# Kernel optimization log

Hardware: AMD Instinct MI355X
Metric: run time of the kernel (lower is better)

## Reference

```python
import jax, jax.numpy as jnp
import numpy as np

N_NODES = 50000
N_EDGES = 1600000
IN_CH = 128
OUT_CH = 32
HEADS = 4
NEG_SLOPE = 0.2

def setup_inputs() -> dict:
    key = jax.random.key(0)
    ks = jax.random.split(key, 6)
    x = jax.random.normal(ks[0], (N_NODES, IN_CH), dtype=jnp.float32)
    edge_index = jax.random.randint(ks[1], (2, N_EDGES), 0, N_NODES, dtype=jnp.int64)
    # GATConv parameters (glorot-ish scale)
    W = jax.random.normal(ks[2], (IN_CH, HEADS * OUT_CH), dtype=jnp.float32) * (1.0 / np.sqrt(IN_CH))
    att_src = jax.random.normal(ks[3], (HEADS, OUT_CH), dtype=jnp.float32) * (1.0 / np.sqrt(OUT_CH))
    att_dst = jax.random.normal(ks[4], (HEADS, OUT_CH), dtype=jnp.float32) * (1.0 / np.sqrt(OUT_CH))
    bias = jnp.zeros((HEADS * OUT_CH,), dtype=jnp.float32)
    return {"x": x, "edge_index": edge_index, "W": W, "att_src": att_src, "att_dst": att_dst, "bias": bias}

def reference(x, edge_index, W, att_src, att_dst, bias):
    N = x.shape[0]
    H, C = att_src.shape
    # PyG default: add self loops
    loop = jnp.arange(N, dtype=edge_index.dtype)
    src = jnp.concatenate([edge_index[0], loop])  # [E+N]
    dst = jnp.concatenate([edge_index[1], loop])  # [E+N]
    # linear projection -> [N, H, C]
    h = (x @ W).reshape(N, H, C)
    # per-node attention contributions [N, H]
    a_src = jnp.einsum('nhc,hc->nh', h, att_src)
    a_dst = jnp.einsum('nhc,hc->nh', h, att_dst)
    # edge-wise logits with LeakyReLU [E', H]
    alpha = jax.nn.leaky_relu(a_src[src] + a_dst[dst], negative_slope=NEG_SLOPE)
    # segment softmax over incoming edges of each dst node
    amax = jax.ops.segment_max(alpha, dst, num_segments=N)
    alpha = jnp.exp(alpha - amax[dst])
    denom = jax.ops.segment_sum(alpha, dst, num_segments=N)
    alpha = alpha / (denom[dst] + 1e-16)
    # weighted scatter-aggregate of source features [N, H, C]
    msg = h[src] * alpha[..., None]
    out = jax.ops.segment_sum(msg, dst, num_segments=N)
    out = out.reshape(N, H * C) + bias  # concat heads + bias
    return out, alpha
```

## Files before the change

### kernel.cpp

```cpp
#include <hip/hip_runtime.h>
#include <math.h>

#define N_NODES 50000
#define N_EDGES 1600000
#define E_TOT   1650000
#define GROWS   32
#define GEMM_BLOCKS ((N_NODES + GROWS - 1) / GROWS)
#define STRIDE  72
#define NBKT    391
#define PPART   450
#define EPB     3556
#define CAP     32

__device__ __forceinline__ unsigned short f2bf(float f) {
    unsigned int b = __float_as_uint(f);
    return (unsigned short)((b + 0x7FFFu + ((b >> 16) & 1u)) >> 16);
}
__device__ __forceinline__ float bf_lo(unsigned int u) {
    return __uint_as_float(u << 16);
}
__device__ __forceinline__ float bf_hi(unsigned int u) {
    return __uint_as_float(u & 0xFFFF0000u);
}

__global__ __launch_bounds__(256) void k_gemm_part(
    const float* __restrict__ x, const float* __restrict__ W,
    const float* __restrict__ att_src, const float* __restrict__ att_dst,
    unsigned short* __restrict__ hbuf16, float* __restrict__ asrc,
    float* __restrict__ adst,
    const int* __restrict__ esrc, const int* __restrict__ edst,
    unsigned int* __restrict__ cells, int* __restrict__ cellCnt)
{
    __shared__ float  xs[GROWS * 128];
    __shared__ float4 Wl[64 * 32];
    __shared__ int    cur[NBKT];
    const int tid = threadIdx.x;

    if (blockIdx.x >= PPART) {
        const int n0 = (blockIdx.x - PPART) * GROWS;

        {
            const float4* xg = (const float4*)x;
            float4* xs4 = (float4*)xs;
            #pragma unroll
            for (int i = 0; i < 4; i++) {
                int idx = tid + 256 * i;
                int row = n0 + (idx >> 5);
                int col = idx & 31;
                row = min(row, N_NODES - 1);
                xs4[idx] = xg[(size_t)row * 32 + col];
            }
        }

        const int ct = tid & 31;
        const int rt = tid >> 5;
        const int rb = rt * 4;

        float acc[4][4];
        #pragma unroll
        for (int r = 0; r < 4; r++)
            #pragma unroll
            for (int q = 0; q < 4; q++) acc[r][q] = 0.f;

        const float4* W4 = (const float4*)W;
        #pragma unroll
        for (int kc = 0; kc < 2; kc++) {
            const float4* Wg = W4 + kc * 2048;
            __syncthreads();
            #pragma unroll
            for (int i = 0; i < 8; i++)
                Wl[tid + 256 * i] = Wg[tid + 256 * i];
            __syncthreads();

            const int kb = kc * 64;
            #pragma unroll 4
            for (int k = 0; k < 64; k++) {
                float4 wv = Wl[k * 32 + ct];
                #pragma unroll
                for (int r = 0; r < 4; r++) {
                    float xr = xs[(rb + r) * 128 + kb + k];
                    acc[r][0] = fmaf(xr, wv.x, acc[r][0]);
                    acc[r][1] = fmaf(xr, wv.y, acc[r][1]);
                    acc[r][2] = fmaf(xr, wv.z, acc[r][2]);
                    acc[r][3] = fmaf(xr, wv.w, acc[r][3]);
                }
            }
        }

        ushort4* h4 = (ushort4*)hbuf16;
        #pragma unroll
        for (int r = 0; r < 4; r++) {
            int row = n0 + rb + r;
            if (row < N_NODES) {
                ushort4 p;
                p.x = f2bf(acc[r][0]); p.y = f2bf(acc[r][1]);
                p.z = f2bf(acc[r][2]); p.w = f2bf(acc[r][3]);
                h4[(size_t)row * 32 + ct] = p;
            }
        }

        const int head = ct >> 3;
        const int c0   = (ct & 7) * 4;
        const float* As = att_src + head * 32 + c0;
        const float* Ad = att_dst + head * 32 + c0;
        float sv[4], dv[4];
        #pragma unroll
        for (int r = 0; r < 4; r++) {
            sv[r] = acc[r][0]*As[0] + acc[r][1]*As[1] + acc[r][2]*As[2] + acc[r][3]*As[3];
            dv[r] = acc[r][0]*Ad[0] + acc[r][1]*Ad[1] + acc[r][2]*Ad[2] + acc[r][3]*Ad[3];
        }
        #pragma unroll
        for (int off = 4; off >= 1; off >>= 1) {
            #pragma unroll
            for (int r = 0; r < 4; r++) {
                sv[r] += __shfl_down(sv[r], off, 8);
                dv[r] += __shfl_down(dv[r], off, 8);
            }
        }
        if ((ct & 7) == 0) {
            #pragma unroll
            for (int r = 0; r < 4; r++) {
                int row = n0 + rb + r;
                if (row < N_NODES) {
                    asrc[row * 4 + head] = sv[r];
                    adst[row * 4 + head] = dv[r];
                }
            }
        }
    } else {
        const int p = blockIdx.x;
        for (int i = tid; i < NBKT; i += 256) cur[i] = 0;
        __syncthreads();

        const int base = p * EPB;
        const int end  = min(base + EPB, N_EDGES);
        unsigned int* myCells = cells + (size_t)p * NBKT * CAP;
        for (int e = base + tid; e < end; e += 256) {
            int d = edst[e];
            int s = esrc[e];
            int bkt = d >> 7;
            int pos = atomicAdd(&cur[bkt], 1);
            if (pos < CAP)
                myCells[bkt * CAP + pos] = ((unsigned int)(d & 127) << 16) | (unsigned int)s;
        }
        __syncthreads();
        for (int i = tid; i < NBKT; i += 256)
            cellCnt[p * NBKT + i] = min(cur[i], CAP);
    }
}

__global__ __launch_bounds__(512) void k_build(
    const unsigned int* __restrict__ cells, const int* __restrict__ cellCnt,
    int* __restrict__ csr, int* __restrict__ cnt)
{
    __shared__ int cur[128];
    __shared__ int scnt[PPART];
    __shared__ __align__(16) int rows[128 * STRIDE];

    const int tid = threadIdx.x;
    const int b   = blockIdx.x;
    const int d0  = b * 128;
    const int ndst = min(128, N_NODES - d0);
    for (int i = tid; i < 128; i += 512) cur[i] = 0;
    for (int i = tid; i < PPART; i += 512) scnt[i] = cellCnt[i * NBKT + b];
    __syncthreads();

    for (int slot = tid; slot < PPART * CAP; slot += 512) {
        int p = slot >> 5;
        int j = slot & 31;
        if (j < scnt[p]) {
            unsigned int v = cells[((size_t)p * NBKT + b) * CAP + j];
            int dlo = (int)(v >> 16);
            int s   = (int)(v & 0xFFFFu);
            int r = atomicAdd(&cur[dlo], 1);
            if (r < STRIDE) rows[dlo * STRIDE + r] = s;
        }
    }
    __syncthreads();

    int4* dst4 = (int4*)(csr + (size_t)d0 * STRIDE);
    const int4* src4 = (const int4*)rows;
    const int n4 = ndst * (STRIDE / 4);
    for (int k = tid; k < n4; k += 512) dst4[k] = src4[k];
    for (int t = tid; t < ndst; t += 512) cnt[d0 + t] = min(cur[t], STRIDE);
}

__global__ __launch_bounds__(64) void k_gather(
    const int* __restrict__ csr, const float4* __restrict__ asrc,
    const float4* __restrict__ adst, const uint4* __restrict__ hbuf4,
    const int* __restrict__ cnt, const float* __restrict__ bias,
    float4* __restrict__ rden, float4* __restrict__ out4)
{
    __shared__ float4 lds_ex[STRIDE + 1];
    __shared__ int    lds_s[STRIDE + 1];

    const int d    = blockIdx.x;
    const int tid  = threadIdx.x;
    const int c    = cnt[d];
    const int ctot = c + 1;
    const float4 b4 = adst[d];
    const int* row = csr + (size_t)d * STRIDE;

    float4 dp = make_float4(0.f, 0.f, 0.f, 0.f);

    for (int i = tid; i < ctot; i += 64) {
        int s = (i < c) ? row[i] : d;
        float4 a4 = asrc[s];
        float l0=a4.x+b4.x, l1=a4.y+b4.y, l2=a4.z+b4.z, l3=a4.w+b4.w;
        l0=fmaxf(l0,0.2f*l0); l1=fmaxf(l1,0.2f*l1);
        l2=fmaxf(l2,0.2f*l2); l3=fmaxf(l3,0.2f*l3);
        float4 ex;
        ex.x=__expf(l0); ex.y=__expf(l1); ex.z=__expf(l2); ex.w=__expf(l3);
        lds_ex[i] = ex;
        lds_s[i]  = s;
        dp.x+=ex.x; dp.y+=ex.y; dp.z+=ex.z; dp.w+=ex.w;
    }

    #pragma unroll
    for (int o = 32; o >= 1; o >>= 1) {
        dp.x += __shfl_down(dp.x, o, 64);
        dp.y += __shfl_down(dp.y, o, 64);
        dp.z += __shfl_down(dp.z, o, 64);
        dp.w += __shfl_down(dp.w, o, 64);
    }
    float rx = 1.0f / (__shfl(dp.x, 0, 64) + 1e-16f);
    float ry = 1.0f / (__shfl(dp.y, 0, 64) + 1e-16f);
    float rz = 1.0f / (__shfl(dp.z, 0, 64) + 1e-16f);
    float rw = 1.0f / (__shfl(dp.w, 0, 64) + 1e-16f);
    if (tid == 0) rden[d] = make_float4(rx, ry, rz, rw);
    __syncthreads();

    const int lane16 = tid & 15;
    const int q      = tid >> 4;
    const int head   = lane16 >> 2;
    const float rh = (head == 0) ? rx : (head == 1) ? ry : (head == 2) ? rz : rw;

    float a0=0.f,a1=0.f,a2=0.f,a3=0.f,a4=0.f,a5=0.f,a6=0.f,a7=0.f;
    for (int j = q; j < ctot; j += 4) {
        float w = ((const float*)&lds_ex[j])[head] * rh;
        int   s = lds_s[j];
        uint4 hv = hbuf4[(size_t)s * 16 + lane16];
        a0 = fmaf(w, bf_lo(hv.x), a0);
        a1 = fmaf(w, bf_hi(hv.x), a1);
        a2 = fmaf(w, bf_lo(hv.y), a2);
        a3 = fmaf(w, bf_hi(hv.y), a3);
        a4 = fmaf(w, bf_lo(hv.z), a4);
        a5 = fmaf(w, bf_hi(hv.z), a5);
        a6 = fmaf(w, bf_lo(hv.w), a6);
        a7 = fmaf(w, bf_hi(hv.w), a7);
    }
    a0 += __shfl_down(a0, 32, 64); a1 += __shfl_down(a1, 32, 64);
    a2 += __shfl_down(a2, 32, 64); a3 += __shfl_down(a3, 32, 64);
    a4 += __shfl_down(a4, 32, 64); a5 += __shfl_down(a5, 32, 64);
    a6 += __shfl_down(a6, 32, 64); a7 += __shfl_down(a7, 32, 64);
    a0 += __shfl_down(a0, 16, 64); a1 += __shfl_down(a1, 16, 64);
    a2 += __shfl_down(a2, 16, 64); a3 += __shfl_down(a3, 16, 64);
    a4 += __shfl_down(a4, 16, 64); a5 += __shfl_down(a5, 16, 64);
    a6 += __shfl_down(a6, 16, 64); a7 += __shfl_down(a7, 16, 64);
    if (tid < 16) {
        float4 bb0 = ((const float4*)bias)[lane16 * 2];
        float4 bb1 = ((const float4*)bias)[lane16 * 2 + 1];
        float4 o0, o1;
        o0.x = a0 + bb0.x; o0.y = a1 + bb0.y; o0.z = a2 + bb0.z; o0.w = a3 + bb0.w;
        o1.x = a4 + bb1.x; o1.y = a5 + bb1.y; o1.z = a6 + bb1.z; o1.w = a7 + bb1.w;
        out4[(size_t)d * 32 + lane16 * 2]     = o0;
        out4[(size_t)d * 32 + lane16 * 2 + 1] = o1;
    }
}

__global__ __launch_bounds__(256) void k_alpha(
    const int* __restrict__ esrc, const int* __restrict__ edst,
    const float4* __restrict__ asrc, const float4* __restrict__ adst,
    const float4* __restrict__ rden, float4* __restrict__ alpha)
{
    int e = blockIdx.x * 256 + threadIdx.x;
    if (e >= E_TOT) return;
    int s, d;
    if (e < N_EDGES) { s = esrc[e]; d = edst[e]; }
    else             { s = e - N_EDGES; d = s; }
    float4 a4 = asrc[s];
    float4 b4 = adst[d];
    float4 r4 = rden[d];
    float l0=a4.x+b4.x, l1=a4.y+b4.y, l2=a4.z+b4.z, l3=a4.w+b4.w;
    l0=fmaxf(l0,0.2f*l0); l1=fmaxf(l1,0.2f*l1);
    l2=fmaxf(l2,0.2f*l2); l3=fmaxf(l3,0.2f*l3);
    float4 w;
    w.x = __expf(l0) * r4.x;
    w.y = __expf(l1) * r4.y;
    w.z = __expf(l2) * r4.z;
    w.w = __expf(l3) * r4.w;
    alpha[e] = w;
}

extern "C" void kernel_launch(void* const* d_in, const int* in_sizes, int n_in,
                              void* d_out, int out_size, void* d_ws, size_t ws_size,
                              hipStream_t stream)
{
    const float* x       = (const float*)d_in[0];
    const int*   ei      = (const int*)d_in[1];
    const float* W       = (const float*)d_in[2];
    const float* att_src = (const float*)d_in[3];
    const float* att_dst = (const float*)d_in[4];
    const float* bias    = (const float*)d_in[5];

    const int* esrc = ei;
    const int* edst = ei + N_EDGES;

    float* out   = (float*)d_out;
    float* alpha = out + (size_t)N_NODES * 128;

    unsigned short* hbuf16 = (unsigned short*)d_ws;
    float* asrc  = (float*)(hbuf16 + (size_t)N_NODES * 128);
    float* adst  = asrc + N_NODES * 4;
    float* rden  = adst + N_NODES * 4;
    int*   cnt   = (int*)(rden + N_NODES * 4);
    int*   csr   = cnt + N_NODES;
    unsigned int* cells = (unsigned int*)(csr + (size_t)N_NODES * STRIDE);
    int*   cellCnt = (int*)(cells + (size_t)PPART * NBKT * CAP);

    k_gemm_part<<<PPART + GEMM_BLOCKS, 256, 0, stream>>>(
        x, W, att_src, att_dst, hbuf16, asrc, adst,
        esrc, edst, cells, cellCnt);

    k_build<<<NBKT, 512, 0, stream>>>(cells, cellCnt, csr, cnt);

    k_gather<<<N_NODES, 64, 0, stream>>>(csr, (const float4*)asrc,
                                         (const float4*)adst,
                                         (const uint4*)hbuf16, cnt, bias,
                                         (float4*)rden, (float4*)out);

    k_alpha<<<(E_TOT + 255) / 256, 256, 0, stream>>>(esrc, edst,
                                                     (const float4*)asrc,
                                                     (const float4*)adst,
                                                     (const float4*)rden,
                                                     (float4*)alpha);
}
```

Baseline: 220.5 us.

## Compute softmax denominators in build, fuse alpha write into gather launch

Measured after the change: 223.4 us. No clear change (+1.4%).

```diff
diff --git a/kernel.cpp b/kernel.cpp
--- a/kernel.cpp
+++ b/kernel.cpp
@@ -11,6 +11,7 @@
 #define PPART   450
 #define EPB     3556
 #define CAP     32
+#define NALPHA  ((E_TOT + 255) / 256)
 
 __device__ __forceinline__ unsigned short f2bf(float f) {
     unsigned int b = __float_as_uint(f);
@@ -62,7 +63,8 @@
             #pragma unroll
             for (int q = 0; q < 4; q++) acc[r][q] = 0.f;
 
-        const float4* W4 = (const float4*)W;
+        const float4* W4  = (const float4*)W;
+        const float4* xs4 = (const float4*)xs;
         #pragma unroll
         for (int kc = 0; kc < 2; kc++) {
             const float4* Wg = W4 + kc * 2048;
@@ -72,17 +74,32 @@
                 Wl[tid + 256 * i] = Wg[tid + 256 * i];
             __syncthreads();
 
-            const int kb = kc * 64;
-            #pragma unroll 4
-            for (int k = 0; k < 64; k++) {
-                float4 wv = Wl[k * 32 + ct];
+            const int kq = kc * 16;
+            #pragma unroll 2
+            for (int k4 = 0; k4 < 16; k4++) {
+                float4 w0 = Wl[(k4 * 4 + 0) * 32 + ct];
+                float4 w1 = Wl[(k4 * 4 + 1) * 32 + ct];
+                float4 w2 = Wl[(k4 * 4 + 2) * 32 + ct];
+                float4 w3 = Wl[(k4 * 4 + 3) * 32 + ct];
                 #pragma unroll
                 for (int r = 0; r < 4; r++) {
-                    float xr = xs[(rb + r) * 128 + kb + k];
-                    acc[r][0] = fmaf(xr, wv.x, acc[r][0]);
-                    acc[r][1] = fmaf(xr, wv.y, acc[r][1]);
-                    acc[r][2] = fmaf(xr, wv.z, acc[r][2]);
-                    acc[r][3] = fmaf(xr, wv.w, acc[r][3]);
+                    float4 xv = xs4[(rb + r) * 32 + kq + k4];
+                    acc[r][0] = fmaf(xv.x, w0.x, acc[r][0]);
+                    acc[r][1] = fmaf(xv.x, w0.y, acc[r][1]);
+                    acc[r][2] = fmaf(xv.x, w0.z, acc[r][2]);
+                    acc[r][3] = fmaf(xv.x, w0.w, acc[r][3]);
+                    acc[r][0] = fmaf(xv.y, w1.x, acc[r][0]);
+                    acc[r][1] = fmaf(xv.y, w1.y, acc[r][1]);
+                    acc[r][2] = fmaf(xv.y, w1.z, acc[r][2]);
+                    acc[r][3] = fmaf(xv.y, w1.w, acc[r][3]);
+                    acc[r][0] = fmaf(xv.z, w2.x, acc[r][0]);
+                    acc[r][1] = fmaf(xv.z, w2.y, acc[r][1]);
+                    acc[r][2] = fmaf(xv.z, w2.z, acc[r][2]);
+                    acc[r][3] = fmaf(xv.z, w2.w, acc[r][3]);
+                    acc[r][0] = fmaf(xv.w, w3.x, acc[r][0]);
+                    acc[r][1] = fmaf(xv.w, w3.y, acc[r][1]);
+                    acc[r][2] = fmaf(xv.w, w3.z, acc[r][2]);
+                    acc[r][3] = fmaf(xv.w, w3.w, acc[r][3]);
                 }
             }
         }
@@ -151,7 +168,8 @@
 
 __global__ __launch_bounds__(512) void k_build(
     const unsigned int* __restrict__ cells, const int* __restrict__ cellCnt,
-    int* __restrict__ csr, int* __restrict__ cnt)
+    const float4* __restrict__ asrc, const float4* __restrict__ adst,
+    int* __restrict__ csr, int* __restrict__ cnt, float4* __restrict__ rden)
 {
     __shared__ int cur[128];
     __shared__ int scnt[PPART];
@@ -183,25 +201,85 @@
     const int n4 = ndst * (STRIDE / 4);
     for (int k = tid; k < n4; k += 512) dst4[k] = src4[k];
     for (int t = tid; t < ndst; t += 512) cnt[d0 + t] = min(cur[t], STRIDE);
-}
-
-__global__ __launch_bounds__(64) void k_gather(
-    const int* __restrict__ csr, const float4* __restrict__ asrc,
+
+    const int g = tid >> 5, l = tid & 31;
+    for (int dd = g; dd < ndst; dd += 16) {
+        const int dn = d0 + dd;
+        const float4 b4 = adst[dn];
+        const int c = min(cur[dd], STRIDE);
+        float4 dp = make_float4(0.f, 0.f, 0.f, 0.f);
+        for (int i = l; i <= c; i += 32) {
+            int s = (i < c) ? rows[dd * STRIDE + i] : dn;
+            float4 a4 = asrc[s];
+            float l0=a4.x+b4.x, l1=a4.y+b4.y, l2=a4.z+b4.z, l3=a4.w+b4.w;
+            l0=fmaxf(l0,0.2f*l0); l1=fmaxf(l1,0.2f*l1);
+            l2=fmaxf(l2,0.2f*l2); l3=fmaxf(l3,0.2f*l3);
+            dp.x += __expf(l0); dp.y += __expf(l1);
+            dp.z += __expf(l2); dp.w += __expf(l3);
+        }
+        #pragma unroll
+        for (int o = 16; o >= 1; o >>= 1) {
+            dp.x += __shfl_down(dp.x, o, 32);
+            dp.y += __shfl_down(dp.y, o, 32);
+            dp.z += __shfl_down(dp.z, o, 32);
+            dp.w += __shfl_down(dp.w, o, 32);
+        }
+        if (l == 0) {
+            float4 r;
+            r.x = 1.0f / (dp.x + 1e-16f);
+            r.y = 1.0f / (dp.y + 1e-16f);
+            r.z = 1.0f / (dp.z + 1e-16f);
+            r.w = 1.0f / (dp.w + 1e-16f);
+            rden[dn] = r;
+        }
+    }
+}
+
+__global__ __launch_bounds__(64) void k_gather_alpha(
+    const int* __restrict__ csr, const int* __restrict__ esrc,
+    const int* __restrict__ edst, const float4* __restrict__ asrc,
     const float4* __restrict__ adst, const uint4* __restrict__ hbuf4,
     const int* __restrict__ cnt, const float* __restrict__ bias,
-    float4* __restrict__ rden, float4* __restrict__ out4)
+    const float4* __restrict__ rden, float4* __restrict__ alpha,
+    float4* __restrict__ out4)
 {
     __shared__ float4 lds_ex[STRIDE + 1];
     __shared__ int    lds_s[STRIDE + 1];
 
-    const int d    = blockIdx.x;
-    const int tid  = threadIdx.x;
+    const int tid = threadIdx.x;
+
+    if (blockIdx.x < NALPHA) {
+        const int base = blockIdx.x * 256;
+        #pragma unroll
+        for (int i = 0; i < 4; i++) {
+            int e = base + i * 64 + tid;
+            if (e < E_TOT) {
+                int s, d;
+                if (e < N_EDGES) { s = esrc[e]; d = edst[e]; }
+                else             { s = e - N_EDGES; d = s; }
+                float4 a4 = asrc[s];
+                float4 b4 = adst[d];
+                float4 r4 = rden[d];
+                float l0=a4.x+b4.x, l1=a4.y+b4.y, l2=a4.z+b4.z, l3=a4.w+b4.w;
+                l0=fmaxf(l0,0.2f*l0); l1=fmaxf(l1,0.2f*l1);
+                l2=fmaxf(l2,0.2f*l2); l3=fmaxf(l3,0.2f*l3);
+                float4 w;
+                w.x = __expf(l0) * r4.x;
+                w.y = __expf(l1) * r4.y;
+                w.z = __expf(l2) * r4.z;
+                w.w = __expf(l3) * r4.w;
+                alpha[e] = w;
+            }
+        }
+        return;
+    }
+
+    const int d    = blockIdx.x - NALPHA;
     const int c    = cnt[d];
     const int ctot = c + 1;
     const float4 b4 = adst[d];
+    const float4 r4 = rden[d];
     const int* row = csr + (size_t)d * STRIDE;
-
-    float4 dp = make_float4(0.f, 0.f, 0.f, 0.f);
 
     for (int i = tid; i < ctot; i += 64) {
         int s = (i < c) ? row[i] : d;
@@ -209,35 +287,23 @@
         float l0=a4.x+b4.x, l1=a4.y+b4.y, l2=a4.z+b4.z, l3=a4.w+b4.w;
         l0=fmaxf(l0,0.2f*l0); l1=fmaxf(l1,0.2f*l1);
         l2=fmaxf(l2,0.2f*l2); l3=fmaxf(l3,0.2f*l3);
-        float4 ex;
-        ex.x=__expf(l0); ex.y=__expf(l1); ex.z=__expf(l2); ex.w=__expf(l3);
-        lds_ex[i] = ex;
+        float4 w;
+        w.x = __expf(l0) * r4.x;
+        w.y = __expf(l1) * r4.y;
+        w.z = __expf(l2) * r4.z;
+        w.w = __expf(l3) * r4.w;
+        lds_ex[i] = w;
         lds_s[i]  = s;
-        dp.x+=ex.x; dp.y+=ex.y; dp.z+=ex.z; dp.w+=ex.w;
-    }
-
-    #pragma unroll
-    for (int o = 32; o >= 1; o >>= 1) {
-        dp.x += __shfl_down(dp.x, o, 64);
-        dp.y += __shfl_down(dp.y, o, 64);
-        dp.z += __shfl_down(dp.z, o, 64);
-        dp.w += __shfl_down(dp.w, o, 64);
-    }
-    float rx = 1.0f / (__shfl(dp.x, 0, 64) + 1e-16f);
-    float ry = 1.0f / (__shfl(dp.y, 0, 64) + 1e-16f);
-    float rz = 1.0f / (__shfl(dp.z, 0, 64) + 1e-16f);
-    float rw = 1.0f / (__shfl(dp.w, 0, 64) + 1e-16f);
-    if (tid == 0) rden[d] = make_float4(rx, ry, rz, rw);
+    }
     __syncthreads();
 
     const int lane16 = tid & 15;
     const int q      = tid >> 4;
     const int head   = lane16 >> 2;
-    const float rh = (head == 0) ? rx : (head == 1) ? ry : (head == 2) ? rz : rw;
 
     float a0=0.f,a1=0.f,a2=0.f,a3=0.f,a4=0.f,a5=0.f,a6=0.f,a7=0.f;
     for (int j = q; j < ctot; j += 4) {
-        float w = ((const float*)&lds_ex[j])[head] * rh;
+        float w = ((const float*)&lds_ex[j])[head];
         int   s = lds_s[j];
         uint4 hv = hbuf4[(size_t)s * 16 + lane16];
         a0 = fmaf(w, bf_lo(hv.x), a0);
@@ -268,30 +334,6 @@
     }
 }
 
-__global__ __launch_bounds__(256) void k_alpha(
-    const int* __restrict__ esrc, const int* __restrict__ edst,
-    const float4* __restrict__ asrc, const float4* __restrict__ adst,
-    const float4* __restrict__ rden, float4* __restrict__ alpha)
-{
-    int e = blockIdx.x * 256 + threadIdx.x;
-    if (e >= E_TOT) return;
-    int s, d;
-    if (e < N_EDGES) { s = esrc[e]; d = edst[e]; }
-    else             { s = e - N_EDGES; d = s; }
-    float4 a4 = asrc[s];
-    float4 b4 = adst[d];
-    float4 r4 = rden[d];
-    float l0=a4.x+b4.x, l1=a4.y+b4.y, l2=a4.z+b4.z, l3=a4.w+b4.w;
-    l0=fmaxf(l0,0.2f*l0); l1=fmaxf(l1,0.2f*l1);
-    l2=fmaxf(l2,0.2f*l2); l3=fmaxf(l3,0.2f*l3);
-    float4 w;
-    w.x = __expf(l0) * r4.x;
-    w.y = __expf(l1) * r4.y;
-    w.z = __expf(l2) * r4.z;
-    w.w = __expf(l3) * r4.w;
-    alpha[e] = w;
-}
-
 extern "C" void kernel_launch(void* const* d_in, const int* in_sizes, int n_in,
                               void* d_out, int out_size, void* d_ws, size_t ws_size,
                               hipStream_t stream)
@@ -322,16 +364,12 @@
         x, W, att_src, att_dst, hbuf16, asrc, adst,
         esrc, edst, cells, cellCnt);
 
-    k_build<<<NBKT, 512, 0, stream>>>(cells, cellCnt, csr, cnt);
-
-    k_gather<<<N_NODES, 64, 0, stream>>>(csr, (const float4*)asrc,
-                                         (const float4*)adst,
-                                         (const uint4*)hbuf16, cnt, bias,
-                                         (float4*)rden, (float4*)out);
-
-    k_alpha<<<(E_TOT + 255) / 256, 256, 0, stream>>>(esrc, edst,
-                                                     (const float4*)asrc,
-                                                     (const float4*)adst,
-                                                     (const float4*)rden,
-                                                     (float4*)alpha);
-}
+    k_build<<<NBKT, 512, 0, stream>>>(cells, cellCnt,
+                                      (const float4*)asrc, (const float4*)adst,
+                                      csr, cnt, (float4*)rden);
+
+    k_gather_alpha<<<NALPHA + N_NODES, 64, 0, stream>>>(
+        csr, esrc, edst, (const float4*)asrc, (const float4*)adst,
+        (const uint4*)hbuf16, cnt, bias, (const float4*)rden,
+        (float4*)alpha, (float4*)out);
+}
```
